# Optimization experiments

Measured on AMD Instinct MI355X. Metric: run time of the kernel, lower is better.

Reference implementation:

```python
import jax, jax.numpy as jnp
import numpy as np

C1, C2 = 32, 16  # first_no_layer, second_no_layer
BN_EPS = 1e-5


def _irr(x, W, b):
    # Faithful port of irregular_convolution.forward.
    # x: [B, S, C, N, K] (torch layout with an extra seq axis).
    # torch: permute(0,1,3,2) then reshape([B, N, C*K]) -- a logical row-major
    # reshape of the transposed tensor (identical semantics in jnp).
    B, S, C, N, K = x.shape
    t = jnp.swapaxes(x, -1, -2).reshape(B, S, N, C * K)
    y = jnp.einsum('bsnm,om->bsno', t, W) + b  # tiny GEMM
    # permute(0,2,1).unsqueeze(-1) -> [B, S, O, N, 1]
    return jnp.moveaxis(y, -1, 2)[..., None]


def _prepare(y, neigh):
    # Faithful port of prepare_data: broadcast node row then masked_select.
    # y: [B, S, C, 1, N]; masked_select with a row-sorted kernel mask is a gather
    # of each node's sorted semantic neighbors: out[...,n,k] = y[...,0,neigh[n,k]].
    v = y[..., 0, :]          # [B, S, C, N]
    return v[..., neigh]      # [B, S, C, N, K]


def setup_inputs() -> dict:
    key = jax.random.key(0)
    ks = jax.random.split(key, 10)
    B, S, N, K = 8, 24, 4096, 9
    inp = {
        'input': jax.random.normal(ks[0], (B, S, N, K), dtype=jnp.float32),
        'neigh': jnp.sort(jax.random.randint(ks[1], (N, K), 0, N), axis=-1).astype(jnp.int32),
        'W1': jax.random.normal(ks[2], (C1, 1 * K), dtype=jnp.float32) * 0.05,
        'b1': jax.random.normal(ks[3], (C1,), dtype=jnp.float32) * 0.05,
        'W2': jax.random.normal(ks[4], (C2, C1 * K), dtype=jnp.float32) * 0.05,
        'b2': jax.random.normal(ks[5], (C2,), dtype=jnp.float32) * 0.05,
        'gamma': jnp.ones((C2,), dtype=jnp.float32),
        'beta': jnp.zeros((C2,), dtype=jnp.float32),
        'W3': jax.random.normal(ks[6], (1, C2 * K), dtype=jnp.float32) * 0.05,
        'b3': jax.random.normal(ks[7], (1,), dtype=jnp.float32) * 0.05,
    }
    return inp


def reference(input, neigh, W1, b1, W2, b2, gamma, beta, W3, b3):
    x = input[:, :, None]                                   # [B,S,1,N,K]
    h = jax.nn.relu(_irr(x, W1, b1))                        # [B,S,32,N,1]
    h = jnp.swapaxes(h, -1, -2)                             # [B,S,32,1,N]
    g = _prepare(h, neigh)                                  # [B,S,32,N,K]
    y = _irr(g, W2, b2)                                     # [B,S,16,N,1]
    # BatchNorm2d (training mode): stats over batch+spatial, per seq step & channel
    mean = jnp.mean(y, axis=(0, 3, 4), keepdims=True)
    var = jnp.var(y, axis=(0, 3, 4), keepdims=True)
    gb = (1, 1, C2, 1, 1)
    y = gamma.reshape(gb) * (y - mean) * jax.lax.rsqrt(var + BN_EPS) + beta.reshape(gb)
    y = jax.nn.relu(y)
    y = jnp.swapaxes(y, -1, -2)                             # [B,S,16,1,N]
    g = _prepare(y, neigh)                                  # [B,S,16,N,K]
    y = jax.nn.relu(_irr(g, W3, b3))                        # [B,S,1,N,1]
    return jnp.squeeze(y, axis=(2, 4))                      # [B,S,N]
```

## Files before the change

### kernel.cpp

```cpp
#include <hip/hip_runtime.h>
#include <hip/hip_bf16.h>

#define NB 8
#define NS 24
#define NN 4096
#define NC1 32
#define NC2 16
#define BN_COUNT 32768.0f

typedef float f32x4 __attribute__((ext_vector_type(4)));
typedef short bf16x8 __attribute__((ext_vector_type(8)));
union U8 { int4 i; bf16x8 b; };
union Q  { uint4 v; unsigned u[4]; };

#define PERM_LO 0x05040100u
#define PERM_HI 0x07060302u

__device__ __forceinline__ unsigned short bfbits(float x) {
    __hip_bfloat16 h = __float2bfloat16(x);
    return *(unsigned short*)&h;
}

__global__ __launch_bounds__(256) void k_l1tab(const float* __restrict__ input,
                                               const float* __restrict__ W1,
                                               const float* __restrict__ b1,
                                               uint4* __restrict__ hp,
                                               const int* __restrict__ neigh,
                                               int* __restrict__ G2M,
                                               int* __restrict__ G3M,
                                               const float* __restrict__ W2,
                                               const float* __restrict__ W3,
                                               __hip_bfloat16* __restrict__ W2B,
                                               __hip_bfloat16* __restrict__ W3B) {
    __shared__ __align__(16) float win[4680];
    __shared__ __align__(16) float corner[72];
    int blk = blockIdx.x;
    if (blk >= 1536) {
        int j = (blk - 1536) * 256 + threadIdx.x;
        if (j < 36864) {
            int j8 = j & 7;
            int tkbl = j >> 3;
            int l = tkbl & 63;
            int tkb = tkbl >> 6;
            int t = tkb / 9, kb = tkb - t * 9;
            int r = t * 16 + (l & 15);
            int k = kb * 32 + ((l >> 4) << 3) + j8;
            int rem = r * 288 + k;
            G2M[j] = neigh[(rem & 4095) * 9 + (rem >> 12)];
        } else if (j < 77824) {
            int t2 = j - 36864;
            int j8 = t2 & 7;
            int tkbl = t2 >> 3;
            int l = tkbl & 63;
            int tkb = tkbl >> 6;
            int t = tkb / 5, kb = tkb - t * 5;
            int r = t * 16 + (l & 15);
            int k = kb * 32 + ((l >> 4) << 3) + j8;
            int rem = r * 144 + k;
            G3M[t2] = (k < 144) ? neigh[(rem & 4095) * 9 + (rem >> 12)] : 0;
        } else if (j < 82432) {
            int jj = j - 77824;
            int kb = jj >> 9;
            int rest = jj & 511;
            int l = rest >> 3, j8 = rest & 7;
            int o = l & 15;
            int k = kb * 32 + ((l >> 4) << 3) + j8;
            W2B[jj] = __float2bfloat16(W2[o * 288 + k]);
        } else {
            int jj = j - 82432;
            int kb = jj >> 9;
            int rest = jj & 511;
            int l = rest >> 3, j8 = rest & 7;
            int o = l & 15;
            int k = kb * 32 + ((l >> 4) << 3) + j8;
            W3B[jj] = __float2bfloat16((o == 0 && k < 144) ? W3[k] : 0.f);
        }
        return;
    }

    int w = blk & 7, bs = blk >> 3;
    int n0 = w * 512;
    const float* A = input + (size_t)bs * 36864;
    int base = n0 * 9;
    int cnt4 = min(4680, 36864 - base) >> 2;
    const float4* A4 = (const float4*)(A + base);
    float4* win4 = (float4*)win;
    for (int j = threadIdx.x; j < cnt4; j += 256) win4[j] = A4[j];
    if (threadIdx.x < 18) ((float4*)corner)[threadIdx.x] = ((const float4*)A)[threadIdx.x];
    __syncthreads();

    for (int i = threadIdx.x; i < 522; i += 256) {
        int j = i / 58, off = i - j * 58;
        int x = j * 4096 + n0;
        int pstart = (x + 8) / 9;
        int pend   = (x + 520) / 9;
        int p = pstart + off;
        if (p >= pend) continue;
        int nf = (p * 9) & 4095;
        float v[9];
        int wb = (nf - n0) * 9 + j;
        if (nf <= 4087) {
#pragma unroll
            for (int m = 0; m < 9; m++) v[m] = win[wb + 9 * m];
        } else {
            int nw = 4096 - nf;
#pragma unroll
            for (int m = 0; m < 9; m++)
                v[m] = (m < nw) ? win[wb + 9 * m]
                                : corner[(nf + m - 4096) * 9 + j + 1];
        }
        float acc[32];
#pragma unroll 4
        for (int c = 0; c < 32; c++) {
            float a = b1[c];
#pragma unroll
            for (int m = 0; m < 9; m++) a = fmaf(v[m], W1[c * 9 + m], a);
            acc[c] = fmaxf(a, 0.f);
        }
#pragma unroll
        for (int pl = 0; pl < 4; pl++) {
            uint4 d;
            d.x = (unsigned)bfbits(acc[pl * 8 + 0]) | ((unsigned)bfbits(acc[pl * 8 + 1]) << 16);
            d.y = (unsigned)bfbits(acc[pl * 8 + 2]) | ((unsigned)bfbits(acc[pl * 8 + 3]) << 16);
            d.z = (unsigned)bfbits(acc[pl * 8 + 4]) | ((unsigned)bfbits(acc[pl * 8 + 5]) << 16);
            d.w = (unsigned)bfbits(acc[pl * 8 + 6]) | ((unsigned)bfbits(acc[pl * 8 + 7]) << 16);
            hp[((size_t)pl * 192 + bs) * NN + p] = d;
        }
    }
}

__global__ __launch_bounds__(512, 4) void k_layer2(const uint4* __restrict__ hp,
                                                   const int4* __restrict__ G2M4,
                                                   const int4* __restrict__ W2B4,
                                                   const float* __restrict__ b2,
                                                   __hip_bfloat16* __restrict__ y2p,
                                                   float* __restrict__ psum,
                                                   float* __restrict__ psq) {
    __shared__ __align__(16) uint4 hl[4096];
    __shared__ float wred[2][8][16];
    int blk = blockIdx.x;
    int pl = blk & 3, bs = blk >> 2;

    int tid = threadIdx.x;
    int l = tid & 63, w = tid >> 6;
    int o = l & 15, q = l >> 4;

    const int4* gp = G2M4 + (size_t)(w * 9) * 128 + l * 2;
    int4 ia = gp[0];
    int4 ib = gp[1];
    U8 bf; bf.i = W2B4[l];

    const uint4* hb = hp + ((size_t)pl * 192 + bs) * NN;
    for (int j = tid; j < 4096; j += 512) hl[j] = hb[j];
    __syncthreads();

    float bb = b2[o];
    float s1 = 0.f, s2 = 0.f;
    __hip_bfloat16* ypl = y2p + (((size_t)(o >> 3) * 192 + bs) * NN) * 8 + (o & 7);

    f32x4 acc[8];
#pragma unroll
    for (int c = 0; c < 8; c++) acc[c] = (f32x4){0.f, 0.f, 0.f, 0.f};

#pragma unroll
    for (int kb = 0; kb < 9; kb++) {
        int4 na, nb; U8 nbf;
        if (kb < 8) {
            na = gp[(kb + 1) * 128];
            nb = gp[(kb + 1) * 128 + 1];
            nbf.i = W2B4[(kb + 1) * 64 + l];
        }
        Q d[8];
        d[0].v = hl[ia.x]; d[1].v = hl[ia.y]; d[2].v = hl[ia.z]; d[3].v = hl[ia.w];
        d[4].v = hl[ib.x]; d[5].v = hl[ib.y]; d[6].v = hl[ib.z]; d[7].v = hl[ib.w];
#pragma unroll
        for (int c = 0; c < 8; c++) {
            const int q2 = c >> 1;
            const unsigned sel = (c & 1) ? PERM_HI : PERM_LO;
            U8 Af;
            Af.i.x = __builtin_amdgcn_perm(d[1].u[q2], d[0].u[q2], sel);
            Af.i.y = __builtin_amdgcn_perm(d[3].u[q2], d[2].u[q2], sel);
            Af.i.z = __builtin_amdgcn_perm(d[5].u[q2], d[4].u[q2], sel);
            Af.i.w = __builtin_amdgcn_perm(d[7].u[q2], d[6].u[q2], sel);
            acc[c] = __builtin_amdgcn_mfma_f32_16x16x32_bf16(Af.b, bf.b, acc[c], 0, 0, 0);
        }
        if (kb < 8) { ia = na; ib = nb; bf = nbf; }
    }

    int rbase = w * 16 + q * 4;
#pragma unroll
    for (int c = 0; c < 8; c++) {
        int C = pl * 8 + c;
#pragma unroll
        for (int i = 0; i < 4; i++) {
            float v = acc[c][i] + bb;
            s1 += v; s2 += v * v;
            int n = C * 128 + rbase + i;
            ypl[(size_t)n * 8] = __float2bfloat16(v);
        }
    }

    s1 += __shfl_xor(s1, 16); s1 += __shfl_xor(s1, 32);
    s2 += __shfl_xor(s2, 16); s2 += __shfl_xor(s2, 32);
    if (l < 16) { wred[0][w][l] = s1; wred[1][w][l] = s2; }
    __syncthreads();
    if (tid < 16) {
        float a = 0.f, b = 0.f;
#pragma unroll
        for (int ww = 0; ww < 8; ww++) { a += wred[0][ww][tid]; b += wred[1][ww][tid]; }
        int srow = (bs % NS) * 16 + tid;
        int col  = (bs / NS) * 4 + pl;
        psum[srow * 32 + col] = a;
        psq [srow * 32 + col] = b;
    }
}

__global__ __launch_bounds__(512, 4) void k_l3bn(const uint4* __restrict__ y2p,
                                                 const int4* __restrict__ G3M4,
                                                 const int4* __restrict__ W3B4,
                                                 const float* __restrict__ psum,
                                                 const float* __restrict__ psq,
                                                 const float* __restrict__ gamma,
                                                 const float* __restrict__ beta,
                                                 const float* __restrict__ b3,
                                                 float* __restrict__ out) {
    __shared__ __align__(16) uint4 zl[4096];
    __shared__ float scl[8], shf[8];
    int blk = blockIdx.x;
    int oct = blk & 1, bs = blk >> 1;
    int s = bs % NS;
    int tid = threadIdx.x;

    if (tid < 256) {
        int jj = tid >> 5, col = tid & 31;
        int row = s * 16 + oct * 8 + jj;
        float sv = psum[row * 32 + col];
        float qv = psq [row * 32 + col];
        for (int off = 16; off; off >>= 1) {
            sv += __shfl_down(sv, off, 32);
            qv += __shfl_down(qv, off, 32);
        }
        if (col == 0) {
            float mean = sv * (1.0f / BN_COUNT);
            float var  = qv * (1.0f / BN_COUNT) - mean * mean;
            float inv  = rsqrtf(var + 1e-5f);
            int o = oct * 8 + jj;
            float scv = gamma[o] * inv;
            scl[jj] = scv;
            shf[jj] = beta[o] - mean * scv;
        }
    }
    __syncthreads();

    float sc[8], sh[8];
#pragma unroll
    for (int jj = 0; jj < 8; jj++) { sc[jj] = scl[jj]; sh[jj] = shf[jj]; }

    int l = tid & 63, w = tid >> 6;
    int o = l & 15, q = l >> 4;

    const int4* gp0 = G3M4 + (size_t)(w * 5) * 128 + l * 2;
    int4 ia = gp0[0];
    int4 ib = gp0[1];
    U8 bf; bf.i = W3B4[l];

    const uint4* yb = y2p + ((size_t)oct * 192 + bs) * NN;
    for (int j = tid; j < 4096; j += 512) {
        uint4 u = yb[j];
        unsigned r[4] = {u.x, u.y, u.z, u.w};
        uint4 pk;
        unsigned* pp = (unsigned*)&pk;
#pragma unroll
        for (int dd = 0; dd < 4; dd++) {
            float lo = fmaxf(fmaf(__uint_as_float(r[dd] << 16),         sc[dd*2],   sh[dd*2]),   0.f);
            float hi = fmaxf(fmaf(__uint_as_float(r[dd] & 0xffff0000u), sc[dd*2+1], sh[dd*2+1]), 0.f);
            unsigned ulo = __float_as_uint(lo) + 0x8000u;
            unsigned uhi = __float_as_uint(hi) + 0x8000u;
            pp[dd] = __builtin_amdgcn_perm(uhi, ulo, PERM_HI);
        }
        zl[j] = pk;
    }
    __syncthreads();

    float b3v = b3[0];

#pragma unroll
    for (int tt = 0; tt < 2; tt++) {
        int t = tt * 8 + w;
        const int4* gp = G3M4 + (size_t)(t * 5) * 128 + l * 2;
        f32x4 acc[8];
#pragma unroll
        for (int c = 0; c < 8; c++) acc[c] = (f32x4){0.f, 0.f, 0.f, 0.f};
#pragma unroll
        for (int kb = 0; kb < 5; kb++) {
            int4 na, nb; U8 nbf;
            if (kb < 4) {
                na = gp[(kb + 1) * 128];
                nb = gp[(kb + 1) * 128 + 1];
                nbf.i = W3B4[(kb + 1) * 64 + l];
            } else if (tt == 0) {
                const int4* gpn = G3M4 + (size_t)((8 + w) * 5) * 128 + l * 2;
                na = gpn[0];
                nb = gpn[1];
                nbf.i = W3B4[l];
            }
            Q d[8];
            d[0].v = zl[ia.x]; d[1].v = zl[ia.y]; d[2].v = zl[ia.z]; d[3].v = zl[ia.w];
            d[4].v = zl[ib.x]; d[5].v = zl[ib.y]; d[6].v = zl[ib.z]; d[7].v = zl[ib.w];
#pragma unroll
            for (int c = 0; c < 8; c++) {
                const int q2 = c >> 1;
                const unsigned sel = (c & 1) ? PERM_HI : PERM_LO;
                U8 Af;
                Af.i.x = __builtin_amdgcn_perm(d[1].u[q2], d[0].u[q2], sel);
                Af.i.y = __builtin_amdgcn_perm(d[3].u[q2], d[2].u[q2], sel);
                Af.i.z = __builtin_amdgcn_perm(d[5].u[q2], d[4].u[q2], sel);
                Af.i.w = __builtin_amdgcn_perm(d[7].u[q2], d[6].u[q2], sel);
                acc[c] = __builtin_amdgcn_mfma_f32_16x16x32_bf16(Af.b, bf.b, acc[c], 0, 0, 0);
            }
            if (kb < 4 || tt == 0) { ia = na; ib = nb; bf = nbf; }
        }
        if (o == 0) {
            int rbase = t * 16 + q * 4;
            float* ob = out + (size_t)bs * NN + oct * 2048;
#pragma unroll
            for (int c = 0; c < 8; c++)
#pragma unroll
                for (int i = 0; i < 4; i++)
                    ob[c * 256 + rbase + i] = fmaxf(acc[c][i] + b3v, 0.f);
        }
    }
}

extern "C" void kernel_launch(void* const* d_in, const int* in_sizes, int n_in,
                              void* d_out, int out_size, void* d_ws, size_t ws_size,
                              hipStream_t stream) {
    const float* input = (const float*)d_in[0];
    const int*   neigh = (const int*)d_in[1];
    const float* W1    = (const float*)d_in[2];
    const float* b1    = (const float*)d_in[3];
    const float* W2    = (const float*)d_in[4];
    const float* b2    = (const float*)d_in[5];
    const float* gamma = (const float*)d_in[6];
    const float* beta  = (const float*)d_in[7];
    const float* W3    = (const float*)d_in[8];
    const float* b3    = (const float*)d_in[9];
    float* out = (float*)d_out;

    char* ws = (char*)d_ws;
    int*            G2M   = (int*)            (ws);
    int*            G3M   = (int*)            (ws + 147456);
    __hip_bfloat16* W2B   = (__hip_bfloat16*) (ws + 311296);
    __hip_bfloat16* W3B   = (__hip_bfloat16*) (ws + 320512);
    uint4*          h     = (uint4*)          (ws + 325632);
    __hip_bfloat16* y2    = (__hip_bfloat16*) (ws + 50657280);
    float*          psum  = (float*)          (ws + 75823104);
    float*          psq   = (float*)          (ws + 75872256);

    k_l1tab<<<1868, 256, 0, stream>>>(input, W1, b1, h,
                                      neigh, G2M, G3M, W2, W3, W2B, W3B);
    k_layer2<<<768, 512, 0, stream>>>(h, (const int4*)G2M, (const int4*)W2B,
                                      b2, y2, psum, psq);
    k_l3bn<<<384, 512, 0, stream>>>((const uint4*)y2, (const int4*)G3M,
                                    (const int4*)W3B, psum, psq,
                                    gamma, beta, b3, out);
}
```

Before: 138.2 us.

## Fuse layer-1 conv into layer-2 kernel via transposed input staging

Layer 1 no longer writes a bf16 hidden tensor (about 50MB) to global memory. A prep kernel now transposes each input tile into a k-major flat layout, and the layer-2 kernel computes the 8 channels it needs for its plane directly into shared memory before the gather-GEMM. This saves the large intermediate write and read but recomputes nothing extra, since each plane computes only its own channels. Block indexing also changes so blocks sharing a bs are spaced apart. The per-thread 9-element loads from flatT are strided, which may hurt coalescing.

```diff
diff --git a/kernel.cpp b/kernel.cpp
--- a/kernel.cpp
+++ b/kernel.cpp
@@ -21,22 +21,19 @@
     return *(unsigned short*)&h;
 }
 
-__global__ __launch_bounds__(256) void k_l1tab(const float* __restrict__ input,
-                                               const float* __restrict__ W1,
-                                               const float* __restrict__ b1,
-                                               uint4* __restrict__ hp,
-                                               const int* __restrict__ neigh,
-                                               int* __restrict__ G2M,
-                                               int* __restrict__ G3M,
-                                               const float* __restrict__ W2,
-                                               const float* __restrict__ W3,
-                                               __hip_bfloat16* __restrict__ W2B,
-                                               __hip_bfloat16* __restrict__ W3B) {
-    __shared__ __align__(16) float win[4680];
-    __shared__ __align__(16) float corner[72];
+__global__ __launch_bounds__(256) void k_prep(const float* __restrict__ input,
+                                              float* __restrict__ flatT,
+                                              const int* __restrict__ neigh,
+                                              int* __restrict__ G2M,
+                                              int* __restrict__ G3M,
+                                              const float* __restrict__ W2,
+                                              const float* __restrict__ W3,
+                                              __hip_bfloat16* __restrict__ W2B,
+                                              __hip_bfloat16* __restrict__ W3B) {
+    __shared__ __align__(16) float tile[9216];
     int blk = blockIdx.x;
-    if (blk >= 1536) {
-        int j = (blk - 1536) * 256 + threadIdx.x;
+    if (blk >= 768) {
+        int j = (blk - 768) * 256 + threadIdx.x;
         if (j < 36864) {
             int j8 = j & 7;
             int tkbl = j >> 3;
@@ -78,68 +75,38 @@
         return;
     }
 
-    int w = blk & 7, bs = blk >> 3;
-    int n0 = w * 512;
-    const float* A = input + (size_t)bs * 36864;
-    int base = n0 * 9;
-    int cnt4 = min(4680, 36864 - base) >> 2;
-    const float4* A4 = (const float4*)(A + base);
-    float4* win4 = (float4*)win;
-    for (int j = threadIdx.x; j < cnt4; j += 256) win4[j] = A4[j];
-    if (threadIdx.x < 18) ((float4*)corner)[threadIdx.x] = ((const float4*)A)[threadIdx.x];
-    __syncthreads();
-
-    for (int i = threadIdx.x; i < 522; i += 256) {
-        int j = i / 58, off = i - j * 58;
-        int x = j * 4096 + n0;
-        int pstart = (x + 8) / 9;
-        int pend   = (x + 520) / 9;
-        int p = pstart + off;
-        if (p >= pend) continue;
-        int nf = (p * 9) & 4095;
-        float v[9];
-        int wb = (nf - n0) * 9 + j;
-        if (nf <= 4087) {
-#pragma unroll
-            for (int m = 0; m < 9; m++) v[m] = win[wb + 9 * m];
-        } else {
-            int nw = 4096 - nf;
-#pragma unroll
-            for (int m = 0; m < 9; m++)
-                v[m] = (m < nw) ? win[wb + 9 * m]
-                                : corner[(nf + m - 4096) * 9 + j + 1];
-        }
-        float acc[32];
-#pragma unroll 4
-        for (int c = 0; c < 32; c++) {
-            float a = b1[c];
-#pragma unroll
-            for (int m = 0; m < 9; m++) a = fmaf(v[m], W1[c * 9 + m], a);
-            acc[c] = fmaxf(a, 0.f);
-        }
-#pragma unroll
-        for (int pl = 0; pl < 4; pl++) {
-            uint4 d;
-            d.x = (unsigned)bfbits(acc[pl * 8 + 0]) | ((unsigned)bfbits(acc[pl * 8 + 1]) << 16);
-            d.y = (unsigned)bfbits(acc[pl * 8 + 2]) | ((unsigned)bfbits(acc[pl * 8 + 3]) << 16);
-            d.z = (unsigned)bfbits(acc[pl * 8 + 4]) | ((unsigned)bfbits(acc[pl * 8 + 5]) << 16);
-            d.w = (unsigned)bfbits(acc[pl * 8 + 6]) | ((unsigned)bfbits(acc[pl * 8 + 7]) << 16);
-            hp[((size_t)pl * 192 + bs) * NN + p] = d;
-        }
-    }
-}
-
-__global__ __launch_bounds__(512, 4) void k_layer2(const uint4* __restrict__ hp,
-                                                   const int4* __restrict__ G2M4,
-                                                   const int4* __restrict__ W2B4,
-                                                   const float* __restrict__ b2,
-                                                   __hip_bfloat16* __restrict__ y2p,
-                                                   float* __restrict__ psum,
-                                                   float* __restrict__ psq) {
+    int bs = blk >> 2, tt = blk & 3;
+    int n0 = tt << 10;
+    const float4* src = (const float4*)(input + (size_t)bs * 36864 + (size_t)n0 * 9);
+    float4* tp = (float4*)tile;
+    for (int j = threadIdx.x; j < 2304; j += 256) tp[j] = src[j];
+    __syncthreads();
+    float* dst = flatT + (size_t)bs * 36864 + n0;
+    for (int j = threadIdx.x; j < 2304; j += 256) {
+        int k = j >> 8, u = j & 255;
+        float4 w;
+        w.x = tile[(u * 4 + 0) * 9 + k];
+        w.y = tile[(u * 4 + 1) * 9 + k];
+        w.z = tile[(u * 4 + 2) * 9 + k];
+        w.w = tile[(u * 4 + 3) * 9 + k];
+        *(float4*)(dst + k * 4096 + u * 4) = w;
+    }
+}
+
+__global__ __launch_bounds__(512, 4) void k_l12(const float* __restrict__ flatT,
+                                                const float* __restrict__ W1,
+                                                const float* __restrict__ b1,
+                                                const int4* __restrict__ G2M4,
+                                                const int4* __restrict__ W2B4,
+                                                const float* __restrict__ b2,
+                                                __hip_bfloat16* __restrict__ y2p,
+                                                float* __restrict__ psum,
+                                                float* __restrict__ psq) {
     __shared__ __align__(16) uint4 hl[4096];
     __shared__ float wred[2][8][16];
     int blk = blockIdx.x;
-    int pl = blk & 3, bs = blk >> 2;
+    int pl = blk / 192;
+    int bs = blk - pl * 192;
 
     int tid = threadIdx.x;
     int l = tid & 63, w = tid >> 6;
@@ -150,8 +117,33 @@
     int4 ib = gp[1];
     U8 bf; bf.i = W2B4[l];
 
-    const uint4* hb = hp + ((size_t)pl * 192 + bs) * NN;
-    for (int j = tid; j < 4096; j += 512) hl[j] = hb[j];
+    const float* T = flatT + (size_t)bs * 36864;
+    const float* W1s = W1 + pl * 72;
+    float b1v[8];
+#pragma unroll
+    for (int c = 0; c < 8; c++) b1v[c] = b1[pl * 8 + c];
+
+#pragma unroll 2
+    for (int j = 0; j < 8; j++) {
+        int p = tid + 512 * j;
+        const float* tp = T + p * 9;
+        float v[9];
+#pragma unroll
+        for (int m = 0; m < 9; m++) v[m] = tp[m];
+        uint4 d;
+        unsigned* dp = (unsigned*)&d;
+#pragma unroll
+        for (int pr = 0; pr < 4; pr++) {
+            float a0 = b1v[2 * pr], a1 = b1v[2 * pr + 1];
+#pragma unroll
+            for (int m = 0; m < 9; m++) a0 = fmaf(v[m], W1s[(2 * pr) * 9 + m], a0);
+#pragma unroll
+            for (int m = 0; m < 9; m++) a1 = fmaf(v[m], W1s[(2 * pr + 1) * 9 + m], a1);
+            dp[pr] = (unsigned)bfbits(fmaxf(a0, 0.f)) |
+                     ((unsigned)bfbits(fmaxf(a1, 0.f)) << 16);
+        }
+        hl[p] = d;
+    }
     __syncthreads();
 
     float bb = b2[o];
@@ -352,15 +344,15 @@
     int*            G3M   = (int*)            (ws + 147456);
     __hip_bfloat16* W2B   = (__hip_bfloat16*) (ws + 311296);
     __hip_bfloat16* W3B   = (__hip_bfloat16*) (ws + 320512);
-    uint4*          h     = (uint4*)          (ws + 325632);
-    __hip_bfloat16* y2    = (__hip_bfloat16*) (ws + 50657280);
-    float*          psum  = (float*)          (ws + 75823104);
-    float*          psq   = (float*)          (ws + 75872256);
-
-    k_l1tab<<<1868, 256, 0, stream>>>(input, W1, b1, h,
-                                      neigh, G2M, G3M, W2, W3, W2B, W3B);
-    k_layer2<<<768, 512, 0, stream>>>(h, (const int4*)G2M, (const int4*)W2B,
-                                      b2, y2, psum, psq);
+    float*          flatT = (float*)          (ws + 325632);
+    __hip_bfloat16* y2    = (__hip_bfloat16*) (ws + 28637184);
+    float*          psum  = (float*)          (ws + 53803008);
+    float*          psq   = (float*)          (ws + 53852160);
+
+    k_prep<<<1100, 256, 0, stream>>>(input, flatT, neigh, G2M, G3M,
+                                     W2, W3, W2B, W3B);
+    k_l12<<<768, 512, 0, stream>>>(flatT, W1, b1, (const int4*)G2M,
+                                   (const int4*)W2B, b2, y2, psum, psq);
     k_l3bn<<<384, 512, 0, stream>>>((const uint4*)y2, (const int4*)G3M,
                                     (const int4*)W3B, psum, psq,
                                     gamma, beta, b3, out);
```

New measurement: 131.9 us (median of 2 runs). 1.05x faster.
